# Kernel tuning notes

Hardware: AMD Instinct MI355X
Metric: run time of the kernel (lower is better)

## Reference

```python
import jax, jax.numpy as jnp
import numpy as np
from jax import lax

B, D, BOND, OUT = 16384, 784, 5, 10

def setup_inputs() -> dict:
    key = jax.random.key(0)
    k = jax.random.split(key, 6)
    x = jax.random.uniform(k[0], (B, D), dtype=jnp.float32)
    core_first = jax.random.normal(k[1], (1, 2, BOND), dtype=jnp.float32) * 0.1
    cores_mid = jax.random.normal(k[2], (D - 2, BOND, 2, BOND), dtype=jnp.float32) * 0.1
    core_last = jax.random.normal(k[3], (BOND, 2, 1), dtype=jnp.float32) * 0.1
    # xavier_uniform for fc.weight with fan_in=1, fan_out=OUT
    bound = float(np.sqrt(6.0 / (1 + OUT)))
    fc_w = jax.random.uniform(k[4], (OUT, 1), dtype=jnp.float32, minval=-bound, maxval=bound)
    fc_b = jnp.zeros((OUT,), dtype=jnp.float32)
    return {"x": x, "core_first": core_first, "cores_mid": cores_mid,
            "core_last": core_last, "fc_w": fc_w, "fc_b": fc_b}

def reference(x, core_first, cores_mid, core_last, fc_w, fc_b):
    # x: [B, D] -> feature map [B, D, 2] = stack(1-x, x)
    xs = jnp.stack([1.0 - x, x], axis=-1)            # [B, D, 2]
    # first core: (1, 2, bond) -> initial carry [B, bond]
    carry0 = jnp.einsum('bi,ir->br', xs[:, 0], core_first[0])  # [B, bond]
    # sequential tensor-train contraction over middle sites via scan
    xs_mid = jnp.moveaxis(xs[:, 1:-1], 1, 0)          # [D-2, B, 2]
    def step(carry, inp):
        xi, core = inp                                # xi: [B,2], core: [bond,2,bond]
        carry = jnp.einsum('bl,bi,lir->br', carry, xi, core)
        return carry, None
    carry, _ = lax.scan(step, carry0, (xs_mid, cores_mid))
    # last core: (bond, 2, 1) -> scalar per batch element
    vlast = jnp.einsum('bi,li->bl', xs[:, -1], core_last[:, :, 0])  # [B, bond]
    res = jnp.sum(carry * vlast, axis=-1, keepdims=True)            # [B, 1]
    out = res @ fc_w.T + fc_b                          # [B, OUT]
    return out
```

## Files before the change

### kernel.cpp

```cpp
#include <hip/hip_runtime.h>


typedef float v2f __attribute__((ext_vector_type(2)));

constexpr int Bn     = 16384;
constexpr int Dn     = 784;
constexpr int NOUT   = 10;
constexpr int NPAIR  = 390;
constexpr int PFV    = 41;
constexpr int PMAT   = 22;
constexpr int BWD_P0 = 349;
constexpr int PKP    = 112;

__device__ __forceinline__ v2f fma2(v2f a, v2f b, v2f c) {
    return __builtin_elementwise_fma(a, b, c);
}
__device__ __forceinline__ v2f sp2(float x) { v2f v = {x, x}; return v; }

struct R5 { v2f a, b; float e; };
struct C5 { v2f a[5], b[5], e01, e23; float e4; };

__device__ __forceinline__ void buildC(const float* __restrict__ s,
                                       float xa, float xb, C5& C) {
    const float xab = xa * xb;
    const v2f va = sp2(xa), vb = sp2(xb), vab = sp2(xab);
#pragma unroll
    for (int l = 0; l < 5; ++l) {
        v2f a = *(const v2f*)(s + 4 * l);
        a = fma2(va,  *(const v2f*)(s + 28 + 4 * l), a);
        a = fma2(vb,  *(const v2f*)(s + 56 + 4 * l), a);
        a = fma2(vab, *(const v2f*)(s + 84 + 4 * l), a);
        C.a[l] = a;
        v2f b = *(const v2f*)(s + 4 * l + 2);
        b = fma2(va,  *(const v2f*)(s + 30 + 4 * l), b);
        b = fma2(vb,  *(const v2f*)(s + 58 + 4 * l), b);
        b = fma2(vab, *(const v2f*)(s + 86 + 4 * l), b);
        C.b[l] = b;
    }
    v2f e01 = *(const v2f*)(s + 20);
    e01 = fma2(va,  *(const v2f*)(s + 48),  e01);
    e01 = fma2(vb,  *(const v2f*)(s + 76),  e01);
    e01 = fma2(vab, *(const v2f*)(s + 104), e01);
    C.e01 = e01;
    v2f e23 = *(const v2f*)(s + 22);
    e23 = fma2(va,  *(const v2f*)(s + 50),  e23);
    e23 = fma2(vb,  *(const v2f*)(s + 78),  e23);
    e23 = fma2(vab, *(const v2f*)(s + 106), e23);
    C.e23 = e23;
    C.e4 = fmaf(xab, s[108], fmaf(xb, s[80], fmaf(xa, s[52], s[24])));
}

__device__ __forceinline__ R5 rowmul(const R5& s, const C5& C) {
    R5 t;
    t.a = sp2(s.a[0]) * C.a[0];
    t.b = sp2(s.a[0]) * C.b[0];
    t.a = fma2(sp2(s.a[1]), C.a[1], t.a); t.b = fma2(sp2(s.a[1]), C.b[1], t.b);
    t.a = fma2(sp2(s.b[0]), C.a[2], t.a); t.b = fma2(sp2(s.b[0]), C.b[2], t.b);
    t.a = fma2(sp2(s.b[1]), C.a[3], t.a); t.b = fma2(sp2(s.b[1]), C.b[3], t.b);
    t.a = fma2(sp2(s.e),    C.a[4], t.a); t.b = fma2(sp2(s.e),    C.b[4], t.b);
    v2f acc = s.a * C.e01;
    acc = fma2(s.b, C.e23, acc);
    t.e = fmaf(s.e, C.e4, acc[0] + acc[1]);
    return t;
}

__global__ void prepack_pairs(const float* __restrict__ cm, float* __restrict__ pk)
{
    int idx = blockIdx.x * 256 + threadIdx.x;
    if (idx >= NPAIR * 100) return;
    int p = idx / 100, rest = idx - p * 100;
    int q = rest / 25, e = rest - q * 25;
    int l = e / 5, r = e - l * 5;
    int m1 = 2 * p + 1, m2 = 2 * p + 2;
    const float* L = cm + (size_t)(m1 * 5 + l) * 10;
    float acc = 0.f;
#pragma unroll
    for (int k = 0; k < 5; ++k) {
        float Lk = (q & 1) ? (L[5 + k] - L[k]) : L[k];
        const float* R = cm + (size_t)(m2 * 5 + k) * 10;
        float Rk = (q & 2) ? (R[5 + r] - R[r]) : R[r];
        acc = fmaf(Lk, Rk, acc);
    }
    int wl = l, wr = r;
    if (p >= BWD_P0) { wl = r; wr = l; }
    int off = (wr < 4) ? (wl * 4 + wr) : (20 + wl);
    pk[(size_t)p * PKP + q * 28 + off] = acc;
}

__global__ __launch_bounds__(1024, 4)
void mps_pair_smem_kernel(const float* __restrict__ x,
                          const float* __restrict__ core_first,
                          const float* __restrict__ cores_mid,
                          const float* __restrict__ core_last,
                          const float* __restrict__ fc_w,
                          const float* __restrict__ fc_b,
                          const float* __restrict__ pk,
                          float* __restrict__ out)
{
    __shared__ float matbuf[14][25][64];
    __shared__ float bv[5][64];

    const int lane = threadIdx.x & 63;
    const int wseg = __builtin_amdgcn_readfirstlane(threadIdx.x >> 6);
    const int row  = blockIdx.x * 64 + lane;
    const float* __restrict__ xr = x + (size_t)row * Dn;
    const v2f* __restrict__ xr2 = (const v2f*)xr;

    R5 fc;

    if (wseg >= 1 && wseg <= 14) {
        const int p0 = PFV + PMAT * (wseg - 1);
        const float* __restrict__ s = pk + (size_t)p0 * PKP;
        R5 M[5];
        M[0] = {{1.f, 0.f}, {0.f, 0.f}, 0.f};
        M[1] = {{0.f, 1.f}, {0.f, 0.f}, 0.f};
        M[2] = {{0.f, 0.f}, {1.f, 0.f}, 0.f};
        M[3] = {{0.f, 0.f}, {0.f, 1.f}, 0.f};
        M[4] = {{0.f, 0.f}, {0.f, 0.f}, 1.f};
        C5 C;
#pragma unroll 1
        for (int i = 0; i < PMAT; ++i) {
            const v2f xv = xr2[p0 + i + 1];
            buildC(s, xv[0], xv[1], C);
#pragma unroll
            for (int r = 0; r < 5; ++r) M[r] = rowmul(M[r], C);
            s += PKP;
        }
#pragma unroll
        for (int r = 0; r < 5; ++r) {
            matbuf[wseg - 1][r * 5 + 0][lane] = M[r].a[0];
            matbuf[wseg - 1][r * 5 + 1][lane] = M[r].a[1];
            matbuf[wseg - 1][r * 5 + 2][lane] = M[r].b[0];
            matbuf[wseg - 1][r * 5 + 3][lane] = M[r].b[1];
            matbuf[wseg - 1][r * 5 + 4][lane] = M[r].e;
        }
    } else if (wseg == 0) {
        const v2f x01 = xr2[0];
        float cl[5], cn[5];
#pragma unroll
        for (int r = 0; r < 5; ++r)
            cl[r] = fmaf(x01[0], core_first[5 + r] - core_first[r], core_first[r]);
        const float* cm0 = cores_mid;
#pragma unroll
        for (int r = 0; r < 5; ++r) {
            float a = 0.f;
#pragma unroll
            for (int l = 0; l < 5; ++l) {
                float mm = fmaf(x01[1], cm0[l * 10 + 5 + r] - cm0[l * 10 + r],
                                cm0[l * 10 + r]);
                a = fmaf(cl[l], mm, a);
            }
            cn[r] = a;
        }
        fc.a = {cn[0], cn[1]}; fc.b = {cn[2], cn[3]}; fc.e = cn[4];
        const float* __restrict__ s = pk;
        C5 C;
#pragma unroll 1
        for (int p = 0; p < PFV; ++p) {
            const v2f xv = xr2[p + 1];
            buildC(s, xv[0], xv[1], C);
            fc = rowmul(fc, C);
            s += PKP;
        }
    } else {
        const v2f xz = xr2[391];
        float vl[5], vn[5];
#pragma unroll
        for (int l = 0; l < 5; ++l)
            vl[l] = fmaf(xz[1], core_last[2 * l + 1] - core_last[2 * l],
                         core_last[2 * l]);
        const float* cmL = cores_mid + (size_t)781 * 50;
#pragma unroll
        for (int l = 0; l < 5; ++l) {
            float a = 0.f;
#pragma unroll
            for (int r = 0; r < 5; ++r) {
                float mm = fmaf(xz[0], cmL[l * 10 + 5 + r] - cmL[l * 10 + r],
                                cmL[l * 10 + r]);
                a = fmaf(mm, vl[r], a);
            }
            vn[l] = a;
        }
        R5 u; u.a = {vn[0], vn[1]}; u.b = {vn[2], vn[3]}; u.e = vn[4];
        const float* __restrict__ s = pk + (size_t)(NPAIR - 1) * PKP;
        C5 C;
#pragma unroll 1
        for (int p = NPAIR - 1; p >= BWD_P0; --p) {
            const v2f xv = xr2[p + 1];
            buildC(s, xv[0], xv[1], C);
            u = rowmul(u, C);
            s -= PKP;
        }
        bv[0][lane] = u.a[0]; bv[1][lane] = u.a[1];
        bv[2][lane] = u.b[0]; bv[3][lane] = u.b[1];
        bv[4][lane] = u.e;
    }

    __syncthreads();

    if (wseg == 0) {
        float cl[5] = {fc.a[0], fc.a[1], fc.b[0], fc.b[1], fc.e};
#pragma unroll 1
        for (int w2 = 0; w2 < 14; ++w2) {
            float v0[5];
#pragma unroll
            for (int r = 0; r < 5; ++r) v0[r] = cl[0] * matbuf[w2][r][lane];
#pragma unroll
            for (int l = 1; l < 5; ++l)
#pragma unroll
                for (int r = 0; r < 5; ++r)
                    v0[r] = fmaf(cl[l], matbuf[w2][l * 5 + r][lane], v0[r]);
#pragma unroll
            for (int r = 0; r < 5; ++r) cl[r] = v0[r];
        }
        float res = 0.f;
#pragma unroll
        for (int l = 0; l < 5; ++l) res = fmaf(cl[l], bv[l][lane], res);
        float* orow = out + (size_t)row * NOUT;
#pragma unroll
        for (int o = 0; o < NOUT; ++o) orow[o] = fmaf(res, fc_w[o], fc_b[o]);
    }
}

extern "C" void kernel_launch(void* const* d_in, const int* in_sizes, int n_in,
                              void* d_out, int out_size, void* d_ws, size_t ws_size,
                              hipStream_t stream) {
    const float* x          = (const float*)d_in[0];
    const float* core_first = (const float*)d_in[1];
    const float* cores_mid  = (const float*)d_in[2];
    const float* core_last  = (const float*)d_in[3];
    const float* fc_w       = (const float*)d_in[4];
    const float* fc_b       = (const float*)d_in[5];
    float* out              = (float*)d_out;
    float* pk               = (float*)d_ws;

    hipLaunchKernelGGL(prepack_pairs, dim3((NPAIR * 100 + 255) / 256), dim3(256),
                       0, stream, cores_mid, pk);
    hipLaunchKernelGGL(mps_pair_smem_kernel, dim3(Bn / 64), dim3(1024), 0, stream,
                       x, core_first, cores_mid, core_last, fc_w, fc_b, pk, out);
}
```

Before: 145.7 us.

## Split tensor-train chain across two blocks per row group with finalize kernel

```diff
diff --git a/kernel.cpp b/kernel.cpp
--- a/kernel.cpp
+++ b/kernel.cpp
@@ -1,68 +1,12 @@
 #include <hip/hip_runtime.h>
 
-
-typedef float v2f __attribute__((ext_vector_type(2)));
 
 constexpr int Bn     = 16384;
 constexpr int Dn     = 784;
 constexpr int NOUT   = 10;
 constexpr int NPAIR  = 390;
-constexpr int PFV    = 41;
-constexpr int PMAT   = 22;
-constexpr int BWD_P0 = 349;
-constexpr int PKP    = 112;
-
-__device__ __forceinline__ v2f fma2(v2f a, v2f b, v2f c) {
-    return __builtin_elementwise_fma(a, b, c);
-}
-__device__ __forceinline__ v2f sp2(float x) { v2f v = {x, x}; return v; }
-
-struct R5 { v2f a, b; float e; };
-struct C5 { v2f a[5], b[5], e01, e23; float e4; };
-
-__device__ __forceinline__ void buildC(const float* __restrict__ s,
-                                       float xa, float xb, C5& C) {
-    const float xab = xa * xb;
-    const v2f va = sp2(xa), vb = sp2(xb), vab = sp2(xab);
-#pragma unroll
-    for (int l = 0; l < 5; ++l) {
-        v2f a = *(const v2f*)(s + 4 * l);
-        a = fma2(va,  *(const v2f*)(s + 28 + 4 * l), a);
-        a = fma2(vb,  *(const v2f*)(s + 56 + 4 * l), a);
-        a = fma2(vab, *(const v2f*)(s + 84 + 4 * l), a);
-        C.a[l] = a;
-        v2f b = *(const v2f*)(s + 4 * l + 2);
-        b = fma2(va,  *(const v2f*)(s + 30 + 4 * l), b);
-        b = fma2(vb,  *(const v2f*)(s + 58 + 4 * l), b);
-        b = fma2(vab, *(const v2f*)(s + 86 + 4 * l), b);
-        C.b[l] = b;
-    }
-    v2f e01 = *(const v2f*)(s + 20);
-    e01 = fma2(va,  *(const v2f*)(s + 48),  e01);
-    e01 = fma2(vb,  *(const v2f*)(s + 76),  e01);
-    e01 = fma2(vab, *(const v2f*)(s + 104), e01);
-    C.e01 = e01;
-    v2f e23 = *(const v2f*)(s + 22);
-    e23 = fma2(va,  *(const v2f*)(s + 50),  e23);
-    e23 = fma2(vb,  *(const v2f*)(s + 78),  e23);
-    e23 = fma2(vab, *(const v2f*)(s + 106), e23);
-    C.e23 = e23;
-    C.e4 = fmaf(xab, s[108], fmaf(xb, s[80], fmaf(xa, s[52], s[24])));
-}
-
-__device__ __forceinline__ R5 rowmul(const R5& s, const C5& C) {
-    R5 t;
-    t.a = sp2(s.a[0]) * C.a[0];
-    t.b = sp2(s.a[0]) * C.b[0];
-    t.a = fma2(sp2(s.a[1]), C.a[1], t.a); t.b = fma2(sp2(s.a[1]), C.b[1], t.b);
-    t.a = fma2(sp2(s.b[0]), C.a[2], t.a); t.b = fma2(sp2(s.b[0]), C.b[2], t.b);
-    t.a = fma2(sp2(s.b[1]), C.a[3], t.a); t.b = fma2(sp2(s.b[1]), C.b[3], t.b);
-    t.a = fma2(sp2(s.e),    C.a[4], t.a); t.b = fma2(sp2(s.e),    C.b[4], t.b);
-    v2f acc = s.a * C.e01;
-    acc = fma2(s.b, C.e23, acc);
-    t.e = fmaf(s.e, C.e4, acc[0] + acc[1]);
-    return t;
-}
+constexpr int PKP    = 100;
+constexpr int BWD_P0 = 375;
 
 __global__ void prepack_pairs(const float* __restrict__ cm, float* __restrict__ pk)
 {
@@ -83,91 +27,117 @@
     }
     int wl = l, wr = r;
     if (p >= BWD_P0) { wl = r; wr = l; }
-    int off = (wr < 4) ? (wl * 4 + wr) : (20 + wl);
-    pk[(size_t)p * PKP + q * 28 + off] = acc;
-}
-
-__global__ __launch_bounds__(1024, 4)
-void mps_pair_smem_kernel(const float* __restrict__ x,
-                          const float* __restrict__ core_first,
-                          const float* __restrict__ cores_mid,
-                          const float* __restrict__ core_last,
-                          const float* __restrict__ fc_w,
-                          const float* __restrict__ fc_b,
-                          const float* __restrict__ pk,
-                          float* __restrict__ out)
+    pk[(size_t)p * PKP + q * 25 + wl * 5 + wr] = acc;
+}
+
+__device__ __forceinline__ void buildC(const float* __restrict__ s,
+                                       float xa, float xb, float C[25]) {
+    const float xab = xa * xb;
+#pragma unroll
+    for (int k = 0; k < 25; ++k) {
+        float t = xab * s[75 + k];
+        t = fmaf(xb, s[50 + k], t);
+        t = fmaf(xa, s[25 + k], t);
+        C[k] = t + s[k];
+    }
+}
+
+__device__ __forceinline__ void vstep(float c[5], const float C[25]) {
+    float t[5];
+#pragma unroll
+    for (int r = 0; r < 5; ++r) t[r] = c[0] * C[r];
+#pragma unroll
+    for (int l = 1; l < 5; ++l)
+#pragma unroll
+        for (int r = 0; r < 5; ++r) t[r] = fmaf(c[l], C[l * 5 + r], t[r]);
+#pragma unroll
+    for (int r = 0; r < 5; ++r) c[r] = t[r];
+}
+
+__device__ __forceinline__ void mstep(float M[25], const float C[25]) {
+#pragma unroll
+    for (int i = 0; i < 5; ++i) {
+        float t[5];
+#pragma unroll
+        for (int r = 0; r < 5; ++r) t[r] = M[i * 5] * C[r];
+#pragma unroll
+        for (int l = 1; l < 5; ++l)
+#pragma unroll
+            for (int r = 0; r < 5; ++r) t[r] = fmaf(M[i * 5 + l], C[l * 5 + r], t[r]);
+#pragma unroll
+        for (int r = 0; r < 5; ++r) M[i * 5 + r] = t[r];
+    }
+}
+
+__global__ __launch_bounds__(1024, 8)
+void mps_half_kernel(const float* __restrict__ x,
+                     const float* __restrict__ core_first,
+                     const float* __restrict__ cores_mid,
+                     const float* __restrict__ core_last,
+                     const float* __restrict__ pk,
+                     float* __restrict__ out)
 {
-    __shared__ float matbuf[14][25][64];
-    __shared__ float bv[5][64];
+    __shared__ float matbuf[8][25][64];
 
     const int lane = threadIdx.x & 63;
     const int wseg = __builtin_amdgcn_readfirstlane(threadIdx.x >> 6);
-    const int row  = blockIdx.x * 64 + lane;
-    const float* __restrict__ xr = x + (size_t)row * Dn;
-    const v2f* __restrict__ xr2 = (const v2f*)xr;
-
-    R5 fc;
-
-    if (wseg >= 1 && wseg <= 14) {
-        const int p0 = PFV + PMAT * (wseg - 1);
+    const int half = blockIdx.x & 1;
+    const int row  = (blockIdx.x >> 1) * 64 + lane;
+    const float*  __restrict__ xr  = x + (size_t)row * Dn;
+    const float2* __restrict__ xr2 = (const float2*)xr;
+
+    const bool isVec = (half == 0) ? (wseg == 0) : (wseg == 15);
+
+    float M[25];
+    float cl[5];
+    float C[25];
+
+    if (!isVec) {
+        const int p0 = (half == 0) ? (15 + 12 * (wseg - 1)) : (195 + 12 * wseg);
         const float* __restrict__ s = pk + (size_t)p0 * PKP;
-        R5 M[5];
-        M[0] = {{1.f, 0.f}, {0.f, 0.f}, 0.f};
-        M[1] = {{0.f, 1.f}, {0.f, 0.f}, 0.f};
-        M[2] = {{0.f, 0.f}, {1.f, 0.f}, 0.f};
-        M[3] = {{0.f, 0.f}, {0.f, 1.f}, 0.f};
-        M[4] = {{0.f, 0.f}, {0.f, 0.f}, 1.f};
-        C5 C;
-#pragma unroll 1
-        for (int i = 0; i < PMAT; ++i) {
-            const v2f xv = xr2[p0 + i + 1];
-            buildC(s, xv[0], xv[1], C);
-#pragma unroll
-            for (int r = 0; r < 5; ++r) M[r] = rowmul(M[r], C);
+#pragma unroll
+        for (int k = 0; k < 25; ++k) M[k] = (k % 6 == 0) ? 1.0f : 0.0f;
+#pragma unroll 1
+        for (int i = 0; i < 12; ++i) {
+            const float2 xv = xr2[p0 + i + 1];
+            buildC(s, xv.x, xv.y, C);
+            mstep(M, C);
             s += PKP;
         }
-#pragma unroll
-        for (int r = 0; r < 5; ++r) {
-            matbuf[wseg - 1][r * 5 + 0][lane] = M[r].a[0];
-            matbuf[wseg - 1][r * 5 + 1][lane] = M[r].a[1];
-            matbuf[wseg - 1][r * 5 + 2][lane] = M[r].b[0];
-            matbuf[wseg - 1][r * 5 + 3][lane] = M[r].b[1];
-            matbuf[wseg - 1][r * 5 + 4][lane] = M[r].e;
-        }
-    } else if (wseg == 0) {
-        const v2f x01 = xr2[0];
-        float cl[5], cn[5];
+    } else if (half == 0) {
+        const float2 x01 = xr2[0];
+        float cn[5];
 #pragma unroll
         for (int r = 0; r < 5; ++r)
-            cl[r] = fmaf(x01[0], core_first[5 + r] - core_first[r], core_first[r]);
+            cl[r] = fmaf(x01.x, core_first[5 + r] - core_first[r], core_first[r]);
         const float* cm0 = cores_mid;
 #pragma unroll
         for (int r = 0; r < 5; ++r) {
             float a = 0.f;
 #pragma unroll
             for (int l = 0; l < 5; ++l) {
-                float mm = fmaf(x01[1], cm0[l * 10 + 5 + r] - cm0[l * 10 + r],
+                float mm = fmaf(x01.y, cm0[l * 10 + 5 + r] - cm0[l * 10 + r],
                                 cm0[l * 10 + r]);
                 a = fmaf(cl[l], mm, a);
             }
             cn[r] = a;
         }
-        fc.a = {cn[0], cn[1]}; fc.b = {cn[2], cn[3]}; fc.e = cn[4];
+#pragma unroll
+        for (int r = 0; r < 5; ++r) cl[r] = cn[r];
         const float* __restrict__ s = pk;
-        C5 C;
-#pragma unroll 1
-        for (int p = 0; p < PFV; ++p) {
-            const v2f xv = xr2[p + 1];
-            buildC(s, xv[0], xv[1], C);
-            fc = rowmul(fc, C);
+#pragma unroll 1
+        for (int p = 0; p < 15; ++p) {
+            const float2 xv = xr2[p + 1];
+            buildC(s, xv.x, xv.y, C);
+            vstep(cl, C);
             s += PKP;
         }
     } else {
-        const v2f xz = xr2[391];
+        const float2 xz = xr2[391];
         float vl[5], vn[5];
 #pragma unroll
         for (int l = 0; l < 5; ++l)
-            vl[l] = fmaf(xz[1], core_last[2 * l + 1] - core_last[2 * l],
+            vl[l] = fmaf(xz.y, core_last[2 * l + 1] - core_last[2 * l],
                          core_last[2 * l]);
         const float* cmL = cores_mid + (size_t)781 * 50;
 #pragma unroll
@@ -175,51 +145,125 @@
             float a = 0.f;
 #pragma unroll
             for (int r = 0; r < 5; ++r) {
-                float mm = fmaf(xz[0], cmL[l * 10 + 5 + r] - cmL[l * 10 + r],
+                float mm = fmaf(xz.x, cmL[l * 10 + 5 + r] - cmL[l * 10 + r],
                                 cmL[l * 10 + r]);
                 a = fmaf(mm, vl[r], a);
             }
             vn[l] = a;
         }
-        R5 u; u.a = {vn[0], vn[1]}; u.b = {vn[2], vn[3]}; u.e = vn[4];
+#pragma unroll
+        for (int l = 0; l < 5; ++l) cl[l] = vn[l];
         const float* __restrict__ s = pk + (size_t)(NPAIR - 1) * PKP;
-        C5 C;
 #pragma unroll 1
         for (int p = NPAIR - 1; p >= BWD_P0; --p) {
-            const v2f xv = xr2[p + 1];
-            buildC(s, xv[0], xv[1], C);
-            u = rowmul(u, C);
+            const float2 xv = xr2[p + 1];
+            buildC(s, xv.x, xv.y, C);
+            vstep(cl, C);
             s -= PKP;
         }
-        bv[0][lane] = u.a[0]; bv[1][lane] = u.a[1];
-        bv[2][lane] = u.b[0]; bv[3][lane] = u.b[1];
-        bv[4][lane] = u.e;
-    }
-
+    }
+
+    if (!isVec && ((half == 0 && wseg <= 8) || (half == 1 && wseg >= 8))) {
+        const int slot = (half == 0) ? (wseg - 1) : (wseg - 8);
+#pragma unroll
+        for (int k = 0; k < 25; ++k) matbuf[slot][k][lane] = M[k];
+    }
     __syncthreads();
 
-    if (wseg == 0) {
-        float cl[5] = {fc.a[0], fc.a[1], fc.b[0], fc.b[1], fc.e};
-#pragma unroll 1
-        for (int w2 = 0; w2 < 14; ++w2) {
-            float v0[5];
-#pragma unroll
-            for (int r = 0; r < 5; ++r) v0[r] = cl[0] * matbuf[w2][r][lane];
-#pragma unroll
-            for (int l = 1; l < 5; ++l)
-#pragma unroll
-                for (int r = 0; r < 5; ++r)
-                    v0[r] = fmaf(cl[l], matbuf[w2][l * 5 + r][lane], v0[r]);
-#pragma unroll
-            for (int r = 0; r < 5; ++r) cl[r] = v0[r];
-        }
-        float res = 0.f;
-#pragma unroll
-        for (int l = 0; l < 5; ++l) res = fmaf(cl[l], bv[l][lane], res);
+    if (isVec) {
+        if (half == 0) {
+#pragma unroll 1
+            for (int s2 = 0; s2 < 8; ++s2) {
+                float t[5];
+#pragma unroll
+                for (int r = 0; r < 5; ++r) t[r] = cl[0] * matbuf[s2][r][lane];
+#pragma unroll
+                for (int l = 1; l < 5; ++l)
+#pragma unroll
+                    for (int r = 0; r < 5; ++r)
+                        t[r] = fmaf(cl[l], matbuf[s2][l * 5 + r][lane], t[r]);
+#pragma unroll
+                for (int r = 0; r < 5; ++r) cl[r] = t[r];
+            }
+        } else {
+#pragma unroll 1
+            for (int s2 = 6; s2 >= 0; --s2) {
+                float t[5];
+#pragma unroll
+                for (int l = 0; l < 5; ++l) {
+                    float a = matbuf[s2][l * 5][lane] * cl[0];
+#pragma unroll
+                    for (int r = 1; r < 5; ++r)
+                        a = fmaf(matbuf[s2][l * 5 + r][lane], cl[r], a);
+                    t[l] = a;
+                }
+#pragma unroll
+                for (int l = 0; l < 5; ++l) cl[l] = t[l];
+            }
+        }
+    }
+    __syncthreads();
+
+    if (!isVec && ((half == 0 && wseg >= 9) || (half == 1 && wseg <= 7))) {
+        const int slot = (half == 0) ? (wseg - 9) : wseg;
+#pragma unroll
+        for (int k = 0; k < 25; ++k) matbuf[slot][k][lane] = M[k];
+    }
+    __syncthreads();
+
+    if (isVec) {
         float* orow = out + (size_t)row * NOUT;
-#pragma unroll
-        for (int o = 0; o < NOUT; ++o) orow[o] = fmaf(res, fc_w[o], fc_b[o]);
-    }
+        if (half == 0) {
+#pragma unroll 1
+            for (int s2 = 0; s2 < 7; ++s2) {
+                float t[5];
+#pragma unroll
+                for (int r = 0; r < 5; ++r) t[r] = cl[0] * matbuf[s2][r][lane];
+#pragma unroll
+                for (int l = 1; l < 5; ++l)
+#pragma unroll
+                    for (int r = 0; r < 5; ++r)
+                        t[r] = fmaf(cl[l], matbuf[s2][l * 5 + r][lane], t[r]);
+#pragma unroll
+                for (int r = 0; r < 5; ++r) cl[r] = t[r];
+            }
+#pragma unroll
+            for (int i = 0; i < 5; ++i) orow[i] = cl[i];
+        } else {
+#pragma unroll 1
+            for (int s2 = 7; s2 >= 0; --s2) {
+                float t[5];
+#pragma unroll
+                for (int l = 0; l < 5; ++l) {
+                    float a = matbuf[s2][l * 5][lane] * cl[0];
+#pragma unroll
+                    for (int r = 1; r < 5; ++r)
+                        a = fmaf(matbuf[s2][l * 5 + r][lane], cl[r], a);
+                    t[l] = a;
+                }
+#pragma unroll
+                for (int l = 0; l < 5; ++l) cl[l] = t[l];
+            }
+#pragma unroll
+            for (int i = 0; i < 5; ++i) orow[5 + i] = cl[i];
+        }
+    }
+}
+
+__global__ __launch_bounds__(256)
+void finalize_kernel(const float* __restrict__ fc_w, const float* __restrict__ fc_b,
+                     float* __restrict__ out)
+{
+    const int row = blockIdx.x * 256 + threadIdx.x;
+    float* o = out + (size_t)row * NOUT;
+    float f[5], g[5];
+#pragma unroll
+    for (int i = 0; i < 5; ++i) { f[i] = o[i]; g[i] = o[5 + i]; }
+    float res = f[0] * g[0];
+#pragma unroll
+    for (int i = 1; i < 5; ++i) res = fmaf(f[i], g[i], res);
+#pragma unroll
+    for (int k = 0; k < NOUT; ++k) o[k] = fmaf(res, fc_w[k], fc_b[k]);
 }
 
 extern "C" void kernel_launch(void* const* d_in, const int* in_sizes, int n_in,
@@ -236,6 +280,8 @@
 
     hipLaunchKernelGGL(prepack_pairs, dim3((NPAIR * 100 + 255) / 256), dim3(256),
                        0, stream, cores_mid, pk);
-    hipLaunchKernelGGL(mps_pair_smem_kernel, dim3(Bn / 64), dim3(1024), 0, stream,
-                       x, core_first, cores_mid, core_last, fc_w, fc_b, pk, out);
-}
+    hipLaunchKernelGGL(mps_half_kernel, dim3(Bn / 64 * 2), dim3(1024), 0, stream,
+                       x, core_first, cores_mid, core_last, pk, out);
+    hipLaunchKernelGGL(finalize_kernel, dim3(Bn / 256), dim3(256), 0, stream,
+                       fc_w, fc_b, out);
+}
```

Result: slower. 170.8 us (+17.2%).
